# Performance work log

Measured on AMD Instinct MI355X. Metric: run time of the kernel, lower is better.

The kernel has to match this reference:

```python
import jax, jax.numpy as jnp
import numpy as np

H = 2048      # hidden_size
I = 8192      # dense intermediate_size
MI = 1024     # moe_intermediate_size
E = 8         # num_local_experts
K = 2         # num_experts_per_tok
B, S = 2, 1024
EPS = 1e-6
ROOT = H ** (-0.5)


def _rms(x, w=None, eps=EPS):
    # fp32 RMSNorm matching _Gemma4CPURMSNorm; w=None -> no-scale variant
    ms = jnp.mean(x * x, axis=-1, keepdims=True) + eps
    y = x * jax.lax.rsqrt(ms)
    return y * w if w is not None else y


def _gelu_tanh(x):
    # gelu_pytorch_tanh == tanh-approximate gelu
    return jax.nn.gelu(x, approximate=True)


def setup_inputs() -> dict:
    key = jax.random.key(0)
    ks = jax.random.split(key, 10)
    s = 0.02
    return {
        "hidden_states": jax.random.normal(ks[0], (B, S, H), jnp.float32),
        # RMSNorm scales (init ones, as in nn.Parameter(torch.ones(dim)))
        "rn_pre1": jnp.ones((H,), jnp.float32),
        "rn_pre2": jnp.ones((H,), jnp.float32),
        "rn_post1": jnp.ones((H,), jnp.float32),
        "rn_post2": jnp.ones((H,), jnp.float32),
        "rn_post": jnp.ones((H,), jnp.float32),
        # dense GLU MLP weights, stored (in, out)
        "w_gate": jax.random.normal(ks[1], (H, I), jnp.float32) * s,
        "w_up":   jax.random.normal(ks[2], (H, I), jnp.float32) * s,
        "w_down": jax.random.normal(ks[3], (I, H), jnp.float32) * s,
        # router
        "router_w": jax.random.normal(ks[4], (H, E), jnp.float32) * s,
        "router_scale": jnp.ones((H,), jnp.float32),
        "per_expert_scale": jnp.ones((E,), jnp.float32),
        # per-expert GLU weights, stacked over experts
        "we_gate": jax.random.normal(ks[5], (E, H, MI), jnp.float32) * s,
        "we_up":   jax.random.normal(ks[6], (E, H, MI), jnp.float32) * s,
        "we_down": jax.random.normal(ks[7], (E, MI, H), jnp.float32) * s,
    }


def reference(hidden_states, rn_pre1, rn_pre2, rn_post1, rn_post2, rn_post,
              w_gate, w_up, w_down, router_w, router_scale, per_expert_scale,
              we_gate, we_up, we_down):
    b, s, h = hidden_states.shape
    T = b * s

    # --- dense branch ---
    dense_in = _rms(hidden_states, rn_pre1)                      # (B,S,H)
    dense_out = (_gelu_tanh(dense_in @ w_gate) * (dense_in @ w_up)) @ w_down
    dense_out = _rms(dense_out, rn_post1)                        # (B,S,H)

    # --- router (takes the raw residual, applies its own no-scale RMSNorm) ---
    x = hidden_states.reshape(T, h)
    xr = _rms(x) * router_scale * ROOT                           # (T,H)
    router_logits = xr @ router_w                                # (T,E)
    probs = jax.nn.softmax(router_logits, axis=-1)
    top_w, top_i = jax.lax.top_k(probs, K)                       # (T,K)
    top_w = top_w / jnp.sum(top_w, axis=-1, keepdims=True)
    top_w = top_w * per_expert_scale[top_i]
    aff = jnp.zeros((T, E), x.dtype).at[jnp.arange(T)[:, None], top_i].set(top_w)

    # --- MoE experts (compute all experts, combine with sparse affinities) ---
    moe_in = _rms(hidden_states, rn_pre2).reshape(T, h)          # (T,H)
    g = jnp.einsum('th,ehm->tem', moe_in, we_gate)               # (T,E,MI)
    u = jnp.einsum('th,ehm->tem', moe_in, we_up)
    eo = jnp.einsum('tem,emh->teh', _gelu_tanh(g) * u, we_down)  # (T,E,H)
    moe_out = jnp.einsum('te,teh->th', aff, eo).reshape(b, s, h)
    moe_out = _rms(moe_out, rn_post2)

    return _rms(dense_out + moe_out, rn_post)
```

## Files before the change

kernel.cpp:

```cpp
#include <hip/hip_runtime.h>
#include <stdint.h>

#define TOK 2048
#define HD  2048
#define ID  8192
#define ID2 16384
#define MID 1024
#define NE  8
#define KSPLIT 4

typedef __attribute__((ext_vector_type(8))) short s16x8;
typedef __attribute__((ext_vector_type(4))) short s16x4;
typedef __attribute__((ext_vector_type(4))) float f32x4;

constexpr float EPSF  = 1e-6f;
constexpr float ROOTF = 0.02209708691207961f;

#define MFMA(a, b, c) __builtin_amdgcn_mfma_f32_16x16x32_bf16(a, b, c, 0, 0, 0)
#define BAR() __builtin_amdgcn_s_barrier()
#define SCHED0() __builtin_amdgcn_sched_barrier(0)
#define VMCNT(n) asm volatile("s_waitcnt vmcnt(" #n ")" ::: "memory")

__device__ __forceinline__ void gload16(const void* g, void* l) {
  __builtin_amdgcn_global_load_lds(
      (const __attribute__((address_space(1))) void*)g,
      (__attribute__((address_space(3))) void*)l, 16, 0, 0);
}

__device__ __forceinline__ short f2bf(float f) {
  union { float f; uint32_t u; } v; v.f = f;
  uint32_t r = v.u + 0x7fffu + ((v.u >> 16) & 1u);
  return (short)(r >> 16);
}

__device__ __forceinline__ float bf2f(short s) {
  union { uint32_t u; float f; } v; v.u = ((uint32_t)(uint16_t)s) << 16;
  return v.f;
}

__device__ __forceinline__ float gelu_tanh(float x) {
  float x3 = x * x * x;
  float u = 0.7978845608028654f * (x + 0.044715f * x3);
  return 0.5f * x * (1.0f + tanhf(u));
}

__global__ __launch_bounds__(256) void k_rms_router(
    const float* __restrict__ x, const float* __restrict__ rnp1,
    const float* __restrict__ rnp2, const float* __restrict__ rsc,
    const float* __restrict__ rw, const float* __restrict__ pes,
    short* __restrict__ rms1, short* __restrict__ rms2,
    int* __restrict__ cnt, int* __restrict__ tokl,
    float* __restrict__ wgtl, int* __restrict__ slotl) {
  const int t = blockIdx.x, tid = threadIdx.x;
  const size_t base = (size_t)t * HD;
  f32x4 v[2];
  float ss = 0.f;
#pragma unroll
  for (int i = 0; i < 2; ++i) {
    v[i] = *(const f32x4*)(x + base + tid * 4 + i * 1024);
#pragma unroll
    for (int j = 0; j < 4; ++j) ss += v[i][j] * v[i][j];
  }
  __shared__ float sr[4];
  __shared__ float sl[32];
#pragma unroll
  for (int off = 32; off; off >>= 1) ss += __shfl_down(ss, off, 64);
  if ((tid & 63) == 0) sr[tid >> 6] = ss;
  __syncthreads();
  const float inv = rsqrtf((sr[0] + sr[1] + sr[2] + sr[3]) * (1.0f / HD) + EPSF);
  float p[8] = {0, 0, 0, 0, 0, 0, 0, 0};
#pragma unroll
  for (int i = 0; i < 2; ++i) {
    const int h = tid * 4 + i * 1024;
    f32x4 w1 = *(const f32x4*)(rnp1 + h);
    f32x4 w2 = *(const f32x4*)(rnp2 + h);
    f32x4 sc = *(const f32x4*)(rsc + h);
    s16x4 o1, o2;
#pragma unroll
    for (int j = 0; j < 4; ++j) {
      float xn = v[i][j] * inv;
      o1[j] = f2bf(xn * w1[j]);
      o2[j] = f2bf(xn * w2[j]);
      float xq = xn * sc[j] * ROOTF;
      const float* rr = rw + (size_t)(h + j) * NE;
      f32x4 ra = *(const f32x4*)rr;
      f32x4 rb = *(const f32x4*)(rr + 4);
      p[0] += xq * ra[0]; p[1] += xq * ra[1]; p[2] += xq * ra[2]; p[3] += xq * ra[3];
      p[4] += xq * rb[0]; p[5] += xq * rb[1]; p[6] += xq * rb[2]; p[7] += xq * rb[3];
    }
    *(s16x4*)(rms1 + base + h) = o1;
    *(s16x4*)(rms2 + base + h) = o2;
  }
#pragma unroll
  for (int e = 0; e < 8; ++e)
#pragma unroll
    for (int off = 32; off; off >>= 1) p[e] += __shfl_down(p[e], off, 64);
  if ((tid & 63) == 0) {
#pragma unroll
    for (int e = 0; e < 8; ++e) sl[(tid >> 6) * 8 + e] = p[e];
  }
  __syncthreads();
  if (tid == 0) {
    float l[8];
#pragma unroll
    for (int e = 0; e < 8; ++e) l[e] = sl[e] + sl[8 + e] + sl[16 + e] + sl[24 + e];
    int i1 = 0;
#pragma unroll
    for (int e = 1; e < 8; ++e) if (l[e] > l[i1]) i1 = e;
    int i2 = (i1 == 0) ? 1 : 0;
#pragma unroll
    for (int e = 0; e < 8; ++e) if (e != i1 && l[e] > l[i2]) i2 = e;
    float p2 = expf(l[i2] - l[i1]);
    float s = 1.0f + p2;
    float w1 = (1.0f / s) * pes[i1];
    float w2 = (p2 / s) * pes[i2];
    int q1 = atomicAdd(&cnt[i1], 1);
    tokl[i1 * TOK + q1] = t; wgtl[i1 * TOK + q1] = w1; slotl[i1 * TOK + q1] = 0;
    int q2 = atomicAdd(&cnt[i2], 1);
    tokl[i2 * TOK + q2] = t; wgtl[i2 * TOK + q2] = w2; slotl[i2 * TOK + q2] = 1;
  }
}

__global__ __launch_bounds__(256) void k_transpose(
    const float* __restrict__ in, short* __restrict__ out, int R, int C) {
  __shared__ float tile[64 * 65];
  const int tid = threadIdx.x;
  const int c0 = blockIdx.x * 64, r0 = blockIdx.y * 64;
  const size_t bo = (size_t)blockIdx.z * R * C;
#pragma unroll
  for (int i = 0; i < 4; ++i) {
    int idx = tid + 256 * i;
    int r = idx >> 4, c4 = idx & 15;
    f32x4 f = *(const f32x4*)(in + bo + (size_t)(r0 + r) * C + c0 + c4 * 4);
#pragma unroll
    for (int j = 0; j < 4; ++j) tile[(c4 * 4 + j) * 65 + r] = f[j];
  }
  __syncthreads();
#pragma unroll
  for (int i = 0; i < 2; ++i) {
    int ch = tid + 256 * i;
    int c = ch >> 3, rs = ch & 7;
    s16x8 o;
#pragma unroll
    for (int q = 0; q < 8; ++q) o[q] = f2bf(tile[c * 65 + rs * 8 + q]);
    *(s16x8*)(out + bo + (size_t)(c0 + c) * R + r0 + rs * 8) = o;
  }
}

__global__ __launch_bounds__(512, 2) void k_gemm256(
    const short* __restrict__ Wt,
    const short* __restrict__ X,
    short* __restrict__ C) {
  __shared__ char lds[2][65536];
  const int tid = threadIdx.x;
  const int lane = tid & 63, wave = tid >> 6;
  const int wr = wave >> 2, wc = wave & 3;
  const int ln15 = lane & 15, l16 = lane >> 4;
  const int m0 = blockIdx.x * 256, t0 = blockIdx.y * 256;
  const int swz = (ln15 & 7) << 4;
  const int srow = tid >> 3;
  const int sslot = ((tid & 7) ^ ((tid >> 3) & 7)) << 4;
  const char* Wb = (const char*)Wt;
  const char* Xb = (const char*)X;
  auto STAGE = [&](int kt, int s) {
#pragma unroll
    for (int c = 0; c < 4; ++c) {
      gload16(Wb + (size_t)(m0 + c * 64 + srow) * 4096 + kt * 128 + sslot,
              &lds[s][c * 8192] + wave * 1024);
      gload16(Xb + (size_t)(t0 + c * 64 + srow) * 4096 + kt * 128 + sslot,
              &lds[s][32768 + c * 8192] + wave * 1024);
    }
  };
  f32x4 acc[8][4];
#pragma unroll
  for (int m = 0; m < 8; ++m)
#pragma unroll
    for (int n = 0; n < 4; ++n) acc[m][n] = (f32x4)0.f;
  const int NT = HD / 64;
  STAGE(0, 0);
  STAGE(1, 1);
  VMCNT(8);
  SCHED0();
  BAR();
#pragma unroll 2
  for (int kt = 0; kt < NT; ++kt) {
    const int s = kt & 1;
    const char* sA = &lds[s][0];
    const char* sB = &lds[s][32768];
#pragma unroll
    for (int mh = 0; mh < 2; ++mh)
#pragma unroll
      for (int ks = 0; ks < 2; ++ks) {
        const int ka = (ks * 64 + l16 * 16) ^ swz;
        s16x8 a[4], b[4];
#pragma unroll
        for (int f = 0; f < 4; ++f)
          a[f] = *(const s16x8*)(sA + (wr * 128 + mh * 64 + f * 16 + ln15) * 128 + ka);
#pragma unroll
        for (int n = 0; n < 4; ++n)
          b[n] = *(const s16x8*)(sB + (wc * 64 + n * 16 + ln15) * 128 + ka);
        __builtin_amdgcn_s_setprio(1);
#pragma unroll
        for (int f = 0; f < 4; ++f)
#pragma unroll
          for (int n = 0; n < 4; ++n)
            acc[mh * 4 + f][n] = MFMA(a[f], b[n], acc[mh * 4 + f][n]);
        __builtin_amdgcn_s_setprio(0);
      }
    BAR();
    if (kt + 2 < NT) {
      STAGE(kt + 2, s);
      VMCNT(8);
    } else if (kt + 1 < NT) {
      VMCNT(0);
    }
    SCHED0();
    BAR();
  }
#pragma unroll
  for (int mi = 0; mi < 8; ++mi)
#pragma unroll
    for (int n = 0; n < 4; ++n) {
      const int t = t0 + wc * 64 + n * 16 + ln15;
      const int i = m0 + wr * 128 + mi * 16 + l16 * 4;
      s16x4 o;
#pragma unroll
      for (int r = 0; r < 4; ++r) o[r] = f2bf(acc[mi][n][r]);
      *(s16x4*)(C + (size_t)t * ID2 + i) = o;
    }
}

__global__ __launch_bounds__(512, 2) void k_dd256(
    const short* __restrict__ Wd,
    const short* __restrict__ X,
    float* __restrict__ dparts) {
  __shared__ char lds[2][65536];
  const int tid = threadIdx.x;
  const int lane = tid & 63, wave = tid >> 6;
  const int wr = wave >> 2, wc = wave & 3;
  const int ln15 = lane & 15, l16 = lane >> 4;
  const int m0 = blockIdx.x * 256, t0 = blockIdx.y * 256;
  const size_t kB = (size_t)blockIdx.z * 4096;
  const int swz = (ln15 & 7) << 4;
  const int srow = tid >> 3;
  const int sslot = ((tid & 7) ^ ((tid >> 3) & 7)) << 4;
  const char* Wb = (const char*)Wd;
  const char* Xb = (const char*)X;
  auto STAGE = [&](int kt, int s) {
#pragma unroll
    for (int c = 0; c < 4; ++c) {
      gload16(Wb + (size_t)(m0 + c * 64 + srow) * 16384 + kB + kt * 128 + sslot,
              &lds[s][c * 8192] + wave * 1024);
      gload16(Xb + (size_t)(t0 + c * 64 + srow) * 16384 + kB + kt * 128 + sslot,
              &lds[s][32768 + c * 8192] + wave * 1024);
    }
  };
  f32x4 acc[8][4];
#pragma unroll
  for (int m = 0; m < 8; ++m)
#pragma unroll
    for (int n = 0; n < 4; ++n) acc[m][n] = (f32x4)0.f;
  const int NT = (ID / KSPLIT) / 64;
  STAGE(0, 0);
  STAGE(1, 1);
  VMCNT(8);
  SCHED0();
  BAR();
#pragma unroll 2
  for (int kt = 0; kt < NT; ++kt) {
    const int s = kt & 1;
    const char* sA = &lds[s][0];
    const char* sB = &lds[s][32768];
#pragma unroll
    for (int mh = 0; mh < 2; ++mh)
#pragma unroll
      for (int ks = 0; ks < 2; ++ks) {
        const int ka = (ks * 64 + l16 * 16) ^ swz;
        s16x8 a[4], b[4];
#pragma unroll
        for (int f = 0; f < 4; ++f)
          a[f] = *(const s16x8*)(sA + (wr * 128 + mh * 64 + f * 16 + ln15) * 128 + ka);
#pragma unroll
        for (int n = 0; n < 4; ++n)
          b[n] = *(const s16x8*)(sB + (wc * 64 + n * 16 + ln15) * 128 + ka);
        __builtin_amdgcn_s_setprio(1);
#pragma unroll
        for (int f = 0; f < 4; ++f)
#pragma unroll
          for (int n = 0; n < 4; ++n)
            acc[mh * 4 + f][n] = MFMA(a[f], b[n], acc[mh * 4 + f][n]);
        __builtin_amdgcn_s_setprio(0);
      }
    BAR();
    if (kt + 2 < NT) {
      STAGE(kt + 2, s);
      VMCNT(8);
    } else if (kt + 1 < NT) {
      VMCNT(0);
    }
    SCHED0();
    BAR();
  }
  float* dst = dparts + (size_t)blockIdx.z * TOK * HD;
#pragma unroll
  for (int mi = 0; mi < 8; ++mi)
#pragma unroll
    for (int n = 0; n < 4; ++n) {
      const int t = t0 + wc * 64 + n * 16 + ln15;
      const int h = m0 + wr * 128 + mi * 16 + l16 * 4;
      *(f32x4*)(dst + (size_t)t * HD + h) = acc[mi][n];
    }
}

__global__ __launch_bounds__(256) void k_gelumul(
    const short* __restrict__ cbuf, short* __restrict__ o) {
  const int flat = blockIdx.x * 256 + threadIdx.x;
  const int t = flat >> 10;
  const int i8 = (flat & 1023) * 8;
  const short* g = cbuf + (size_t)t * ID2 + i8;
  s16x8 gv = *(const s16x8*)g;
  s16x8 uv = *(const s16x8*)(g + ID);
  s16x8 ov;
#pragma unroll
  for (int j = 0; j < 8; ++j)
    ov[j] = f2bf(gelu_tanh(bf2f(gv[j])) * bf2f(uv[j]));
  *(s16x8*)(o + (size_t)t * ID + i8) = ov;
}

__global__ __launch_bounds__(256) void k_exp_gateup(
    const short* __restrict__ wegT, const short* __restrict__ weuT,
    const short* __restrict__ rms2,
    const int* __restrict__ cnt, const int* __restrict__ tokl,
    short* __restrict__ acte) {
  const int e = blockIdx.z;
  const int cn = cnt[e];
  const int t0 = blockIdx.y * 128;
  if (t0 >= cn) return;
  const int n0 = blockIdx.x * 64;
  __shared__ short sW[128 * 32];
  __shared__ short sX[128 * 32];
  const int tid = threadIdx.x;
  const int lane = tid & 63, wave = tid >> 6;
  const int ln15 = lane & 15, k8 = (lane >> 4) * 8;
  const int nsub = (wave & 1) * 32, tsub = (wave >> 1) * 64;
  const int srow = tid >> 2, skc = (tid & 3) * 8;
  const int* tl = tokl + e * TOK;
  int r0 = t0 + srow, r1 = t0 + 64 + srow;
  int tk0 = tl[r0 < cn ? r0 : cn - 1];
  int tk1 = tl[r1 < cn ? r1 : cn - 1];
  const short* gW0 = wegT + (size_t)e * MID * HD + (size_t)(n0 + srow) * HD + skc;
  const short* gW1 = weuT + (size_t)e * MID * HD + (size_t)(n0 + srow) * HD + skc;
  const short* gX0 = rms2 + (size_t)tk0 * HD + skc;
  const short* gX1 = rms2 + (size_t)tk1 * HD + skc;
  char* lW = (char*)sW + wave * 1024;
  char* lX = (char*)sX + wave * 1024;
  f32x4 accg[2][4], accu[2][4];
#pragma unroll
  for (int m = 0; m < 2; ++m)
#pragma unroll
    for (int n = 0; n < 4; ++n) { accg[m][n] = (f32x4)0.f; accu[m][n] = (f32x4)0.f; }
  for (int kt = 0; kt < HD / 32; ++kt) {
    const int ko = kt * 32;
    __syncthreads();
    gload16(gW0 + ko, lW);
    gload16(gW1 + ko, lW + 4096);
    gload16(gX0 + ko, lX);
    gload16(gX1 + ko, lX + 4096);
    __syncthreads();
    s16x8 ag[2], au[2], bx[4];
#pragma unroll
    for (int m = 0; m < 2; ++m) {
      ag[m] = *(const s16x8*)(sW + (nsub + m * 16 + ln15) * 32 + k8);
      au[m] = *(const s16x8*)(sW + (64 + nsub + m * 16 + ln15) * 32 + k8);
    }
#pragma unroll
    for (int n = 0; n < 4; ++n)
      bx[n] = *(const s16x8*)(sX + (tsub + n * 16 + ln15) * 32 + k8);
#pragma unroll
    for (int m = 0; m < 2; ++m)
#pragma unroll
      for (int n = 0; n < 4; ++n) {
        accg[m][n] = MFMA(ag[m], bx[n], accg[m][n]);
        accu[m][n] = MFMA(au[m], bx[n], accu[m][n]);
      }
  }
#pragma unroll
  for (int m = 0; m < 2; ++m)
#pragma unroll
    for (int n = 0; n < 4; ++n) {
      const int r = t0 + tsub + n * 16 + ln15;
      if (r < cn) {
        const int ib = n0 + nsub + m * 16 + (lane >> 4) * 4;
        s16x4 o;
#pragma unroll
        for (int q = 0; q < 4; ++q)
          o[q] = f2bf(gelu_tanh(accg[m][n][q]) * accu[m][n][q]);
        *(s16x4*)(acte + (size_t)e * TOK * MID + (size_t)r * MID + ib) = o;
      }
    }
}

__global__ __launch_bounds__(256) void k_exp_down(
    const short* __restrict__ wedT,
    const short* __restrict__ acte,
    const int* __restrict__ cnt, const int* __restrict__ tokl,
    const float* __restrict__ wgtl, const int* __restrict__ slotl,
    float* __restrict__ moep) {
  const int e = blockIdx.z;
  const int cn = cnt[e];
  const int t0 = blockIdx.y * 128;
  if (t0 >= cn) return;
  const int n0 = blockIdx.x * 128;
  __shared__ short sW[128 * 32];
  __shared__ short sX[128 * 32];
  const int tid = threadIdx.x;
  const int lane = tid & 63, wave = tid >> 6;
  const int wr = wave >> 1, wc = wave & 1;
  const int ln15 = lane & 15, k8 = (lane >> 4) * 8;
  const int srow = tid >> 2, skc = (tid & 3) * 8;
  const short* wb = wedT + (size_t)e * HD * MID;
  const short* gW0 = wb + (size_t)(n0 + srow) * MID + skc;
  const short* gW1 = wb + (size_t)(n0 + 64 + srow) * MID + skc;
  const short* ab = acte + (size_t)e * TOK * MID;
  const short* gX0 = ab + (size_t)(t0 + srow) * MID + skc;
  const short* gX1 = ab + (size_t)(t0 + 64 + srow) * MID + skc;
  char* lW = (char*)sW + wave * 1024;
  char* lX = (char*)sX + wave * 1024;
  f32x4 acc[4][4];
#pragma unroll
  for (int m = 0; m < 4; ++m)
#pragma unroll
    for (int n = 0; n < 4; ++n) acc[m][n] = (f32x4)0.f;
  for (int kt = 0; kt < MID / 32; ++kt) {
    const int ko = kt * 32;
    __syncthreads();
    gload16(gW0 + ko, lW);
    gload16(gW1 + ko, lW + 4096);
    gload16(gX0 + ko, lX);
    gload16(gX1 + ko, lX + 4096);
    __syncthreads();
    s16x8 a[4], b[4];
#pragma unroll
    for (int m = 0; m < 4; ++m)
      a[m] = *(const s16x8*)(sW + (wr * 64 + m * 16 + ln15) * 32 + k8);
#pragma unroll
    for (int n = 0; n < 4; ++n)
      b[n] = *(const s16x8*)(sX + (wc * 64 + n * 16 + ln15) * 32 + k8);
#pragma unroll
    for (int m = 0; m < 4; ++m)
#pragma unroll
      for (int n = 0; n < 4; ++n) acc[m][n] = MFMA(a[m], b[n], acc[m][n]);
  }
#pragma unroll
  for (int n = 0; n < 4; ++n) {
    const int r = t0 + wc * 64 + n * 16 + ln15;
    if (r < cn) {
      const int tk = tokl[e * TOK + r];
      const float wf = wgtl[e * TOK + r];
      const int sl = slotl[e * TOK + r];
      float* dst = moep + (size_t)sl * TOK * HD + (size_t)tk * HD;
#pragma unroll
      for (int m = 0; m < 4; ++m) {
        const int h = n0 + wr * 64 + m * 16 + (lane >> 4) * 4;
        f32x4 v = acc[m][n] * wf;
        *(f32x4*)(dst + h) = v;
      }
    }
  }
}

__global__ __launch_bounds__(256) void k_final(
    const float* __restrict__ dparts, const float* __restrict__ moep,
    const float* __restrict__ rno1, const float* __restrict__ rno2,
    const float* __restrict__ rnof, float* __restrict__ out) {
  const int t = blockIdx.x, tid = threadIdx.x;
  const size_t base = (size_t)t * HD;
  f32x4 dv[2], mv[2];
  float ssd = 0.f, ssm = 0.f;
#pragma unroll
  for (int i = 0; i < 2; ++i) {
    const int h = tid * 4 + i * 1024;
    dv[i] = (f32x4)0.f;
#pragma unroll
    for (int z = 0; z < KSPLIT; ++z)
      dv[i] += *(const f32x4*)(dparts + (size_t)z * TOK * HD + base + h);
    f32x4 a = *(const f32x4*)(moep + base + h);
    f32x4 b = *(const f32x4*)(moep + (size_t)TOK * HD + base + h);
    mv[i] = a + b;
#pragma unroll
    for (int j = 0; j < 4; ++j) { ssd += dv[i][j] * dv[i][j]; ssm += mv[i][j] * mv[i][j]; }
  }
  __shared__ float sr[8];
#pragma unroll
  for (int off = 32; off; off >>= 1) {
    ssd += __shfl_down(ssd, off, 64);
    ssm += __shfl_down(ssm, off, 64);
  }
  if ((tid & 63) == 0) { sr[tid >> 6] = ssd; sr[4 + (tid >> 6)] = ssm; }
  __syncthreads();
  const float invd = rsqrtf((sr[0] + sr[1] + sr[2] + sr[3]) * (1.0f / HD) + EPSF);
  const float invm = rsqrtf((sr[4] + sr[5] + sr[6] + sr[7]) * (1.0f / HD) + EPSF);
  f32x4 y[2];
  float ssy = 0.f;
#pragma unroll
  for (int i = 0; i < 2; ++i) {
    const int h = tid * 4 + i * 1024;
    f32x4 w1 = *(const f32x4*)(rno1 + h);
    f32x4 w2 = *(const f32x4*)(rno2 + h);
#pragma unroll
    for (int j = 0; j < 4; ++j) {
      y[i][j] = dv[i][j] * invd * w1[j] + mv[i][j] * invm * w2[j];
      ssy += y[i][j] * y[i][j];
    }
  }
  __syncthreads();
#pragma unroll
  for (int off = 32; off; off >>= 1) ssy += __shfl_down(ssy, off, 64);
  if ((tid & 63) == 0) sr[tid >> 6] = ssy;
  __syncthreads();
  const float invy = rsqrtf((sr[0] + sr[1] + sr[2] + sr[3]) * (1.0f / HD) + EPSF);
#pragma unroll
  for (int i = 0; i < 2; ++i) {
    const int h = tid * 4 + i * 1024;
    f32x4 w = *(const f32x4*)(rnof + h);
    f32x4 o;
#pragma unroll
    for (int j = 0; j < 4; ++j) o[j] = y[i][j] * invy * w[j];
    *(f32x4*)(out + base + h) = o;
  }
}

extern "C" void kernel_launch(void* const* d_in, const int* in_sizes, int n_in,
                              void* d_out, int out_size, void* d_ws, size_t ws_size,
                              hipStream_t stream) {
  (void)in_sizes; (void)n_in; (void)out_size;
  const float* x    = (const float*)d_in[0];
  const float* rnp1 = (const float*)d_in[1];
  const float* rnp2 = (const float*)d_in[2];
  const float* rno1 = (const float*)d_in[3];
  const float* rno2 = (const float*)d_in[4];
  const float* rnof = (const float*)d_in[5];
  const float* wg   = (const float*)d_in[6];
  const float* wu   = (const float*)d_in[7];
  const float* wd   = (const float*)d_in[8];
  const float* rw   = (const float*)d_in[9];
  const float* rsc  = (const float*)d_in[10];
  const float* pes  = (const float*)d_in[11];
  const float* weg  = (const float*)d_in[12];
  const float* weu  = (const float*)d_in[13];
  const float* wed  = (const float*)d_in[14];
  float* out = (float*)d_out;

  char* ws = (char*)d_ws;
  size_t off = 0;
  auto alloc = [&](size_t bytes) -> void* {
    void* p = ws + off;
    off += (bytes + 255) & ~(size_t)255;
    return p;
  };
  const size_t IH  = (size_t)ID * HD;
  const size_t EMH = (size_t)NE * MID * HD;
  short* wgT   = (short*)alloc(IH * 2);
  short* wuT   = (short*)alloc(IH * 2);
  short* wdT   = (short*)alloc(IH * 2);
  short* wegT  = (short*)alloc(EMH * 2);
  short* weuT  = (short*)alloc(EMH * 2);
  short* wedT  = (short*)alloc(EMH * 2);
  short* rms1  = (short*)alloc((size_t)TOK * HD * 2);
  short* rms2  = (short*)alloc((size_t)TOK * HD * 2);
  short* actb  = (short*)alloc((size_t)TOK * ID * 2);
  short* acte  = (short*)alloc((size_t)NE * TOK * MID * 2);
  float* moep  = (float*)alloc((size_t)2 * TOK * HD * 4);
  int*   cnt   = (int*)alloc(NE * 4);
  int*   tokl  = (int*)alloc((size_t)NE * TOK * 4);
  float* wgtl  = (float*)alloc((size_t)NE * TOK * 4);
  int*   slotl = (int*)alloc((size_t)NE * TOK * 4);
  if (off > ws_size) return;
  float* dparts = (float*)wgT;
  short* cbuf = acte;

  hipMemsetAsync(cnt, 0, NE * 4, stream);
  k_rms_router<<<TOK, 256, 0, stream>>>(x, rnp1, rnp2, rsc, rw, pes,
                                        rms1, rms2, cnt, tokl, wgtl, slotl);
  k_transpose<<<dim3(ID / 64, HD / 64, 1), 256, 0, stream>>>(wg, wgT, HD, ID);
  k_transpose<<<dim3(ID / 64, HD / 64, 1), 256, 0, stream>>>(wu, wuT, HD, ID);
  k_transpose<<<dim3(HD / 64, ID / 64, 1), 256, 0, stream>>>(wd, wdT, ID, HD);
  k_transpose<<<dim3(MID / 64, HD / 64, NE), 256, 0, stream>>>(weg, wegT, HD, MID);
  k_transpose<<<dim3(MID / 64, HD / 64, NE), 256, 0, stream>>>(weu, weuT, HD, MID);
  k_transpose<<<dim3(HD / 64, MID / 64, NE), 256, 0, stream>>>(wed, wedT, MID, HD);
  k_gemm256<<<dim3(ID2 / 256, TOK / 256), 512, 0, stream>>>(wgT, rms1, cbuf);
  k_gelumul<<<(TOK * ID) / (256 * 8), 256, 0, stream>>>(cbuf, actb);
  k_dd256<<<dim3(HD / 256, TOK / 256, KSPLIT), 512, 0, stream>>>(wdT, actb, dparts);
  k_exp_gateup<<<dim3(MID / 64, TOK / 128, NE), 256, 0, stream>>>(wegT, weuT, rms2,
                                                                  cnt, tokl, acte);
  k_exp_down<<<dim3(HD / 128, TOK / 128, NE), 256, 0, stream>>>(wedT, acte, cnt, tokl,
                                                                wgtl, slotl, moep);
  k_final<<<TOK, 256, 0, stream>>>(dparts, moep, rno1, rno2, rnof, out);
}
```

Measured before the change: 551.5 us.

## Fuse gate/up weight transpose and bf16 conversion into the GEMM A-load

Drops the two separate transpose kernels for the dense gate and up weights. The gate/up GEMM now reads the fp32 weights directly through registers, converts them to bf16 and writes them swizzled into LDS, while the token tile still goes through direct global-to-LDS loads. The LDS fragment loop is also reordered so B fragments are loaded once per k-step rather than once per m-half, in both GEMMs. This removes a full read/write pass over the gate and up weights. In exchange the A-tile staging now uses VGPRs and strided per-column global reads, and the pipeline waits with vmcnt(0), which weakens overlap.

Result: slower. 757.0 us (+37.2%).

```diff
diff --git a/kernel.cpp b/kernel.cpp
--- a/kernel.cpp
+++ b/kernel.cpp
@@ -20,6 +20,7 @@
 #define BAR() __builtin_amdgcn_s_barrier()
 #define SCHED0() __builtin_amdgcn_sched_barrier(0)
 #define VMCNT(n) asm volatile("s_waitcnt vmcnt(" #n ")" ::: "memory")
+#define LGKM0() asm volatile("s_waitcnt lgkmcnt(0)" ::: "memory")
 
 __device__ __forceinline__ void gload16(const void* g, void* l) {
   __builtin_amdgcn_global_load_lds(
@@ -147,8 +148,9 @@
   }
 }
 
-__global__ __launch_bounds__(512, 2) void k_gemm256(
-    const short* __restrict__ Wt,
+__global__ __launch_bounds__(512, 2) void k_fgu(
+    const float* __restrict__ wg,
+    const float* __restrict__ wu,
     const short* __restrict__ X,
     short* __restrict__ C) {
   __shared__ char lds[2][65536];
@@ -160,16 +162,34 @@
   const int swz = (ln15 & 7) << 4;
   const int srow = tid >> 3;
   const int sslot = ((tid & 7) ^ ((tid >> 3) & 7)) << 4;
-  const char* Wb = (const char*)Wt;
   const char* Xb = (const char*)X;
-  auto STAGE = [&](int kt, int s) {
-#pragma unroll
-    for (int c = 0; c < 4; ++c) {
-      gload16(Wb + (size_t)(m0 + c * 64 + srow) * 4096 + kt * 128 + sslot,
-              &lds[s][c * 8192] + wave * 1024);
+  const float* Wsrc = (m0 < ID) ? wg : wu;
+  const int am = tid & 255;
+  const int mcol = (m0 & (ID - 1)) + am;
+  const int ksl = (tid >> 8) * 4;
+  const int awb = am * 128;
+  float av[4][8];
+  auto LOADA = [&](int kt) {
+#pragma unroll
+    for (int u = 0; u < 4; ++u)
+#pragma unroll
+      for (int j = 0; j < 8; ++j)
+        av[u][j] = Wsrc[(size_t)(kt * 64 + (ksl + u) * 8 + j) * ID + mcol];
+  };
+  auto WRITEA = [&](int s) {
+#pragma unroll
+    for (int u = 0; u < 4; ++u) {
+      s16x8 o;
+#pragma unroll
+      for (int j = 0; j < 8; ++j) o[j] = f2bf(av[u][j]);
+      *(s16x8*)(&lds[s][awb + (((ksl + u) * 16) ^ ((am & 7) << 4))]) = o;
+    }
+  };
+  auto BSTAGE = [&](int kt, int s) {
+#pragma unroll
+    for (int c = 0; c < 4; ++c)
       gload16(Xb + (size_t)(t0 + c * 64 + srow) * 4096 + kt * 128 + sslot,
               &lds[s][32768 + c * 8192] + wave * 1024);
-    }
   };
   f32x4 acc[8][4];
 #pragma unroll
@@ -177,9 +197,13 @@
 #pragma unroll
     for (int n = 0; n < 4; ++n) acc[m][n] = (f32x4)0.f;
   const int NT = HD / 64;
-  STAGE(0, 0);
-  STAGE(1, 1);
-  VMCNT(8);
+  LOADA(0);
+  BSTAGE(0, 0);
+  WRITEA(0);
+  LOADA(1);
+  BSTAGE(1, 1);
+  LGKM0();
+  VMCNT(0);
   SCHED0();
   BAR();
 #pragma unroll 2
@@ -188,17 +212,18 @@
     const char* sA = &lds[s][0];
     const char* sB = &lds[s][32768];
 #pragma unroll
-    for (int mh = 0; mh < 2; ++mh)
-#pragma unroll
-      for (int ks = 0; ks < 2; ++ks) {
-        const int ka = (ks * 64 + l16 * 16) ^ swz;
-        s16x8 a[4], b[4];
+    for (int ks = 0; ks < 2; ++ks) {
+      const int ka = (ks * 64 + l16 * 16) ^ swz;
+      s16x8 b[4];
+#pragma unroll
+      for (int n = 0; n < 4; ++n)
+        b[n] = *(const s16x8*)(sB + (wc * 64 + n * 16 + ln15) * 128 + ka);
+#pragma unroll
+      for (int mh = 0; mh < 2; ++mh) {
+        s16x8 a[4];
 #pragma unroll
         for (int f = 0; f < 4; ++f)
           a[f] = *(const s16x8*)(sA + (wr * 128 + mh * 64 + f * 16 + ln15) * 128 + ka);
-#pragma unroll
-        for (int n = 0; n < 4; ++n)
-          b[n] = *(const s16x8*)(sB + (wc * 64 + n * 16 + ln15) * 128 + ka);
         __builtin_amdgcn_s_setprio(1);
 #pragma unroll
         for (int f = 0; f < 4; ++f)
@@ -207,12 +232,16 @@
             acc[mh * 4 + f][n] = MFMA(a[f], b[n], acc[mh * 4 + f][n]);
         __builtin_amdgcn_s_setprio(0);
       }
+    }
     BAR();
+    if (kt + 1 < NT) {
+      WRITEA(s ^ 1);
+      LGKM0();
+    }
+    VMCNT(0);
     if (kt + 2 < NT) {
-      STAGE(kt + 2, s);
-      VMCNT(8);
-    } else if (kt + 1 < NT) {
-      VMCNT(0);
+      LOADA(kt + 2);
+      BSTAGE(kt + 2, s);
     }
     SCHED0();
     BAR();
@@ -272,17 +301,18 @@
     const char* sA = &lds[s][0];
     const char* sB = &lds[s][32768];
 #pragma unroll
-    for (int mh = 0; mh < 2; ++mh)
-#pragma unroll
-      for (int ks = 0; ks < 2; ++ks) {
-        const int ka = (ks * 64 + l16 * 16) ^ swz;
-        s16x8 a[4], b[4];
+    for (int ks = 0; ks < 2; ++ks) {
+      const int ka = (ks * 64 + l16 * 16) ^ swz;
+      s16x8 b[4];
+#pragma unroll
+      for (int n = 0; n < 4; ++n)
+        b[n] = *(const s16x8*)(sB + (wc * 64 + n * 16 + ln15) * 128 + ka);
+#pragma unroll
+      for (int mh = 0; mh < 2; ++mh) {
+        s16x8 a[4];
 #pragma unroll
         for (int f = 0; f < 4; ++f)
           a[f] = *(const s16x8*)(sA + (wr * 128 + mh * 64 + f * 16 + ln15) * 128 + ka);
-#pragma unroll
-        for (int n = 0; n < 4; ++n)
-          b[n] = *(const s16x8*)(sB + (wc * 64 + n * 16 + ln15) * 128 + ka);
         __builtin_amdgcn_s_setprio(1);
 #pragma unroll
         for (int f = 0; f < 4; ++f)
@@ -291,6 +321,7 @@
             acc[mh * 4 + f][n] = MFMA(a[f], b[n], acc[mh * 4 + f][n]);
         __builtin_amdgcn_s_setprio(0);
       }
+    }
     BAR();
     if (kt + 2 < NT) {
       STAGE(kt + 2, s);
@@ -582,13 +613,11 @@
   hipMemsetAsync(cnt, 0, NE * 4, stream);
   k_rms_router<<<TOK, 256, 0, stream>>>(x, rnp1, rnp2, rsc, rw, pes,
                                         rms1, rms2, cnt, tokl, wgtl, slotl);
-  k_transpose<<<dim3(ID / 64, HD / 64, 1), 256, 0, stream>>>(wg, wgT, HD, ID);
-  k_transpose<<<dim3(ID / 64, HD / 64, 1), 256, 0, stream>>>(wu, wuT, HD, ID);
   k_transpose<<<dim3(HD / 64, ID / 64, 1), 256, 0, stream>>>(wd, wdT, ID, HD);
   k_transpose<<<dim3(MID / 64, HD / 64, NE), 256, 0, stream>>>(weg, wegT, HD, MID);
   k_transpose<<<dim3(MID / 64, HD / 64, NE), 256, 0, stream>>>(weu, weuT, HD, MID);
   k_transpose<<<dim3(HD / 64, MID / 64, NE), 256, 0, stream>>>(wed, wedT, MID, HD);
-  k_gemm256<<<dim3(ID2 / 256, TOK / 256), 512, 0, stream>>>(wgT, rms1, cbuf);
+  k_fgu<<<dim3(ID2 / 256, TOK / 256), 512, 0, stream>>>(wg, wu, rms1, cbuf);
   k_gelumul<<<(TOK * ID) / (256 * 8), 256, 0, stream>>>(cbuf, actb);
   k_dd256<<<dim3(HD / 256, TOK / 256, KSPLIT), 512, 0, stream>>>(wdT, actb, dparts);
   k_exp_gateup<<<dim3(MID / 64, TOK / 128, NE), 256, 0, stream>>>(wegT, weuT, rms2,
```
